# Kernel optimization log

Measured on AMD Instinct MI355X. Metric: run time of the kernel, lower is better.

## Reference

```python
import jax, jax.numpy as jnp
import numpy as np

NUM_HEADS = 8

def setup_inputs() -> dict:
    key = jax.random.key(0)
    ks = jax.random.split(key, 7)
    B, S, H = 2, 4096, 512
    sc = 1.0 / np.sqrt(H)
    x = jax.random.normal(ks[0], (B, S, H), dtype=jnp.float32)
    Wq = jax.random.normal(ks[1], (H, H), dtype=jnp.float32) * sc
    bq = jnp.zeros((H,), dtype=jnp.float32)
    Wk = jax.random.normal(ks[2], (H, H), dtype=jnp.float32) * sc
    bk = jnp.zeros((H,), dtype=jnp.float32)
    Wv = jax.random.normal(ks[3], (H, H), dtype=jnp.float32) * sc
    bv = jnp.zeros((H,), dtype=jnp.float32)
    return {"x": x, "Wq": Wq, "bq": bq, "Wk": Wk, "bk": bk, "Wv": Wv, "bv": bv}

def reference(x, Wq, bq, Wk, bk, Wv, bv):
    B, S, H = x.shape
    hd = H // NUM_HEADS
    def split_heads(t):  # [B,S,H] -> [B,nh,S,hd]
        return t.reshape(B, S, NUM_HEADS, hd).transpose(0, 2, 1, 3)
    q = split_heads(x @ Wq + bq)
    k = split_heads(x @ Wk + bk)
    v = split_heads(x @ Wv + bv)
    scores = jnp.einsum('bhqd,bhkd->bhqk', q, k) / jnp.sqrt(jnp.float32(hd))
    attn = jax.nn.softmax(scores, axis=-1)  # dropout is identity at inference
    out = jnp.einsum('bhqk,bhkd->bhqd', attn, v)
    return out.transpose(0, 2, 1, 3).reshape(B, S, H)
```

## Files before the change

### kernel.cpp

```cpp
#include <hip/hip_runtime.h>
#include <hip/hip_bf16.h>

typedef __attribute__((ext_vector_type(8))) short short8;
typedef __attribute__((ext_vector_type(4))) float float4v;
typedef __attribute__((ext_vector_type(16))) float f32x16;

using bf16 = __hip_bfloat16;

#define QSCALE 0.18033688011112042f

__device__ inline float fexp2(float x) { return __builtin_amdgcn_exp2f(x); }

__device__ inline short f2bf(float f) {
  __hip_bfloat16 h = __float2bfloat16(f);
  short s;
  __builtin_memcpy(&s, &h, 2);
  return s;
}

__device__ inline float4v mfma16(short8 a, short8 b, float4v c) {
  return __builtin_amdgcn_mfma_f32_16x16x32_bf16(a, b, c, 0, 0, 0);
}
__device__ inline f32x16 mfma32(short8 a, short8 b, f32x16 c) {
  return __builtin_amdgcn_mfma_f32_32x32x16_bf16(a, b, c, 0, 0, 0);
}
__device__ inline unsigned pk2(float lo, float hi) {
  __hip_bfloat16 l = __float2bfloat16(lo), h = __float2bfloat16(hi);
  unsigned short ls, hs;
  __builtin_memcpy(&ls, &l, 2);
  __builtin_memcpy(&hs, &h, 2);
  return (unsigned)ls | ((unsigned)hs << 16);
}


__global__ __launch_bounds__(256) void conv_x_kernel(const float* __restrict__ x,
                                                     bf16* __restrict__ xb) {
  int i = blockIdx.x * 256 + threadIdx.x;
  const float4v* src = reinterpret_cast<const float4v*>(x);
  float4v a = src[(size_t)i * 2];
  float4v c = src[(size_t)i * 2 + 1];
  short8 o;
  o[0] = f2bf(a[0]); o[1] = f2bf(a[1]); o[2] = f2bf(a[2]); o[3] = f2bf(a[3]);
  o[4] = f2bf(c[0]); o[5] = f2bf(c[1]); o[6] = f2bf(c[2]); o[7] = f2bf(c[3]);
  *reinterpret_cast<short8*>(xb + (size_t)i * 8) = o;
}

__global__ void conv_w_kernel(const float* __restrict__ Wq, const float* __restrict__ Wk,
                              const float* __restrict__ Wv, bf16* __restrict__ wt) {
  __shared__ float tile[32][33];
  int z = blockIdx.z;
  const float* W = (z == 0) ? Wq : (z == 1) ? Wk : Wv;
  int n = blockIdx.x * 32 + threadIdx.x;
  int k = blockIdx.y * 32 + threadIdx.y;
  tile[threadIdx.y][threadIdx.x] = W[(size_t)k * 512 + n];
  __syncthreads();
  int nn = blockIdx.x * 32 + threadIdx.y;
  int kk = blockIdx.y * 32 + threadIdx.x;
  wt[(size_t)z * 512 * 512 + (size_t)nn * 512 + kk] = __float2bfloat16(tile[threadIdx.x][threadIdx.y]);
}


__global__ __launch_bounds__(256) void qkv_gemm_kernel(
    const bf16* __restrict__ xb, const bf16* __restrict__ wt,
    const float* __restrict__ bq, const float* __restrict__ bk, const float* __restrict__ bv,
    bf16* __restrict__ qb, bf16* __restrict__ kbuf, bf16* __restrict__ vt) {
  __shared__ bf16 Xs[64][72];
  __shared__ bf16 Ws[64][72];
  const int m0 = blockIdx.x * 64;
  const int n0 = blockIdx.y * 64;
  const int z  = blockIdx.z;
  const bf16* W = wt + (size_t)z * 512 * 512;
  const float* bias = (z == 0) ? bq : (z == 1) ? bk : bv;
  const int t = threadIdx.x;
  const int lane = t & 63, wv = t >> 6;
  const int row = t >> 3, col8 = (t & 7) * 8;
  const int lo = lane & 15, g8 = (lane >> 4) * 8;
  float4v acc[4] = {};
  for (int k0 = 0; k0 < 512; k0 += 64) {
    *reinterpret_cast<short8*>(&Xs[row][col8])      = *reinterpret_cast<const short8*>(&xb[(size_t)(m0 + row) * 512 + k0 + col8]);
    *reinterpret_cast<short8*>(&Xs[row + 32][col8]) = *reinterpret_cast<const short8*>(&xb[(size_t)(m0 + row + 32) * 512 + k0 + col8]);
    *reinterpret_cast<short8*>(&Ws[row][col8])      = *reinterpret_cast<const short8*>(&W[(size_t)(n0 + row) * 512 + k0 + col8]);
    *reinterpret_cast<short8*>(&Ws[row + 32][col8]) = *reinterpret_cast<const short8*>(&W[(size_t)(n0 + row + 32) * 512 + k0 + col8]);
    __syncthreads();
    short8 a0 = *reinterpret_cast<const short8*>(&Xs[wv * 16 + lo][g8]);
    short8 a1 = *reinterpret_cast<const short8*>(&Xs[wv * 16 + lo][32 + g8]);
#pragma unroll
    for (int nt = 0; nt < 4; ++nt) {
      short8 b0 = *reinterpret_cast<const short8*>(&Ws[nt * 16 + lo][g8]);
      short8 b1 = *reinterpret_cast<const short8*>(&Ws[nt * 16 + lo][32 + g8]);
      acc[nt] = mfma16(a0, b0, acc[nt]);
      acc[nt] = mfma16(a1, b1, acc[nt]);
    }
    __syncthreads();
  }
#pragma unroll
  for (int nt = 0; nt < 4; ++nt) {
    int ncol = n0 + nt * 16 + lo;
    float bias_v = bias[ncol];
    int h = ncol >> 6, d = ncol & 63;
#pragma unroll
    for (int r = 0; r < 4; ++r) {
      int mrow = m0 + wv * 16 + (lane >> 4) * 4 + r;
      int bb = mrow >> 12, s = mrow & 4095;
      float v = acc[nt][r] + bias_v;
      size_t base = (size_t)(bb * 8 + h) * 262144;
      if (z == 2) {
        size_t idx = (size_t)((d >> 5) * 256 + (s >> 4)) * 512 + (d & 31) * 8 + ((s >> 3) & 1) * 256 + (s & 7);
        vt[base + idx] = __float2bfloat16(v);
      } else {
        size_t idx = (size_t)((s >> 5) * 4 + (d >> 4)) * 512 + (s & 31) * 8 + ((d >> 3) & 1) * 256 + (d & 7);
        if (z == 0) qb[base + idx] = __float2bfloat16(v * QSCALE);
        else        kbuf[base + idx] = __float2bfloat16(v);
      }
    }
  }
}


__device__ __forceinline__ void load_tiles(const bf16* __restrict__ kb2, const bf16* __restrict__ vb2,
                                           int tl, short8 (&kf)[2][4], short8 (&vf)[2][4]) {
#pragma unroll
  for (int c = 0; c < 2; ++c)
#pragma unroll
    for (int ds = 0; ds < 4; ++ds)
      kf[c][ds] = *reinterpret_cast<const short8*>(kb2 + ((size_t)(tl * 2 + c) * 4 + ds) * 512);
#pragma unroll
  for (int dt = 0; dt < 2; ++dt)
#pragma unroll
    for (int gs = 0; gs < 4; ++gs)
      vf[dt][gs] = *reinterpret_cast<const short8*>(vb2 + (size_t)(dt * 256 + tl * 4 + gs) * 512);
}

__device__ __forceinline__ void attn_step(const short8 (&kf)[2][4], const short8 (&vf)[2][4],
                                          const short8 (&qf)[4], f32x16& ot0, f32x16& ot1,
                                          float& l_run, int half) {
  f32x16 p0 = {}, p1 = {};
#pragma unroll
  for (int ds = 0; ds < 4; ++ds) {
    p0 = mfma32(kf[0][ds], qf[ds], p0);
    p1 = mfma32(kf[1][ds], qf[ds], p1);
  }

  float s0 = 0.f, s1 = 0.f, s2 = 0.f, s3 = 0.f;
#pragma unroll
  for (int r = 0; r < 16; r += 4) {
    p0[r]     = fexp2(p0[r]);     s0 += p0[r];
    p0[r + 1] = fexp2(p0[r + 1]); s1 += p0[r + 1];
    p0[r + 2] = fexp2(p0[r + 2]); s2 += p0[r + 2];
    p0[r + 3] = fexp2(p0[r + 3]); s3 += p0[r + 3];
  }
#pragma unroll
  for (int r = 0; r < 16; r += 4) {
    p1[r]     = fexp2(p1[r]);     s0 += p1[r];
    p1[r + 1] = fexp2(p1[r + 1]); s1 += p1[r + 1];
    p1[r + 2] = fexp2(p1[r + 2]); s2 += p1[r + 2];
    p1[r + 3] = fexp2(p1[r + 3]); s3 += p1[r + 3];
  }
  l_run += (s0 + s1) + (s2 + s3);

  unsigned pa[2][2][4];
#pragma unroll
  for (int c = 0; c < 2; ++c) {
    const f32x16& pc = c ? p1 : p0;
    unsigned w[4][2];
#pragma unroll
    for (int cq = 0; cq < 4; ++cq) {
      w[cq][0] = pk2(pc[4 * cq],     pc[4 * cq + 1]);
      w[cq][1] = pk2(pc[4 * cq + 2], pc[4 * cq + 3]);
    }
#pragma unroll
    for (int s = 0; s < 2; ++s)
#pragma unroll
      for (int x = 0; x < 2; ++x) {
        unsigned u = w[2 * s][x], v = w[2 * s + 1][x];
        unsigned pu = __shfl_xor(u, 32), pv = __shfl_xor(v, 32);
        pa[c][s][x]     = half ? pv : u;
        pa[c][s][2 + x] = half ? v  : pu;
      }
  }

#pragma unroll
  for (int c = 0; c < 2; ++c)
#pragma unroll
    for (int s = 0; s < 2; ++s) {
      short8 pb;
      __builtin_memcpy(&pb, pa[c][s], 16);
      ot0 = mfma32(vf[0][c * 2 + s], pb, ot0);
      ot1 = mfma32(vf[1][c * 2 + s], pb, ot1);
    }
}

__global__ __launch_bounds__(256, 1) void attn_kernel(
    const bf16* __restrict__ qbuf, const bf16* __restrict__ kbuf,
    const bf16* __restrict__ vtbuf, float* __restrict__ out) {
  int bid = blockIdx.x;
  int sw = (bid & 7) * 32 + (bid >> 3);
  int bh = sw >> 4, qt = sw & 15;
  const int bI = bh >> 3, hh = bh & 7;
  const int t = threadIdx.x;
  const int wid = t >> 6, lane = t & 63;
  const int l31 = lane & 31, half = lane >> 5;
  const int q0 = qt * 256 + wid * 64;

  const bf16* kb2 = kbuf + (size_t)bh * 262144 + lane * 8;
  const bf16* vb2 = vtbuf + (size_t)bh * 262144 + lane * 8;

  short8 qf0[4], qf1[4];
#pragma unroll
  for (int ds = 0; ds < 4; ++ds) {
    qf0[ds] = *reinterpret_cast<const short8*>(qbuf + (size_t)bh * 262144 + (size_t)(((q0 >> 5) + 0) * 4 + ds) * 512 + lane * 8);
    qf1[ds] = *reinterpret_cast<const short8*>(qbuf + (size_t)bh * 262144 + (size_t)(((q0 >> 5) + 1) * 4 + ds) * 512 + lane * 8);
  }

  f32x16 oa0 = {}, oa1 = {}, ob0 = {}, ob1 = {};
  float lA = 0.f, lB = 0.f;

  short8 kfA[2][4], vfA[2][4], kfB[2][4], vfB[2][4];
  load_tiles(kb2, vb2, 0, kfA, vfA);
  for (int it = 0; it < 64; it += 2) {
    load_tiles(kb2, vb2, it + 1, kfB, vfB);
    attn_step(kfA, vfA, qf0, oa0, oa1, lA, half);
    attn_step(kfA, vfA, qf1, ob0, ob1, lB, half);
    load_tiles(kb2, vb2, (it + 2) & 63, kfA, vfA);
    attn_step(kfB, vfB, qf0, oa0, oa1, lA, half);
    attn_step(kfB, vfB, qf1, ob0, ob1, lB, half);
  }

  lA += __shfl_xor(lA, 32);
  lB += __shfl_xor(lB, 32);

  float invA = 1.0f / lA, invB = 1.0f / lB;
#pragma unroll
  for (int set = 0; set < 2; ++set) {
    const f32x16& t0 = set ? ob0 : oa0;
    const f32x16& t1 = set ? ob1 : oa1;
    float inv = set ? invB : invA;
    int q = q0 + set * 32 + l31;
    float* obase = out + ((size_t)bI * 4096 + q) * 512 + hh * 64;
#pragma unroll
    for (int cq = 0; cq < 4; ++cq) {
      float4v o0, o1;
#pragma unroll
      for (int rr = 0; rr < 4; ++rr) {
        o0[rr] = t0[4 * cq + rr] * inv;
        o1[rr] = t1[4 * cq + rr] * inv;
      }
      *reinterpret_cast<float4v*>(obase + 8 * cq + 4 * half) = o0;
      *reinterpret_cast<float4v*>(obase + 32 + 8 * cq + 4 * half) = o1;
    }
  }
}


extern "C" void kernel_launch(void* const* d_in, const int* in_sizes, int n_in,
                              void* d_out, int out_size, void* d_ws, size_t ws_size,
                              hipStream_t stream) {
  const float* x  = (const float*)d_in[0];
  const float* Wq = (const float*)d_in[1];
  const float* bq = (const float*)d_in[2];
  const float* Wk = (const float*)d_in[3];
  const float* bk = (const float*)d_in[4];
  const float* Wv = (const float*)d_in[5];
  const float* bv = (const float*)d_in[6];
  float* out = (float*)d_out;

  char* ws = (char*)d_ws;
  bf16* xb = (bf16*)(ws + 0);
  bf16* wt = (bf16*)(ws + 8388608);
  bf16* qb = (bf16*)(ws + 9961472);
  bf16* kb = (bf16*)(ws + 18350080);
  bf16* vt = (bf16*)(ws + 26738688);

  conv_x_kernel<<<2048, 256, 0, stream>>>(x, xb);
  conv_w_kernel<<<dim3(16, 16, 3), dim3(32, 32), 0, stream>>>(Wq, Wk, Wv, wt);
  qkv_gemm_kernel<<<dim3(128, 8, 3), 256, 0, stream>>>(xb, wt, bq, bk, bv, qb, kb, vt);
  attn_kernel<<<256, 256, 0, stream>>>(qb, kb, vt, out);
}
```

Baseline: 146.8 us.

## Stage K/V tiles through LDS with double-buffered direct global-to-LDS loads

Replaces per-wave redundant global loads of K and V tiles with a cooperative staging scheme: each of the four waves copies a quarter of the tile into shared memory using global_load_lds, double-buffered across iterations with a barrier per tile. Waves then read fragments from LDS. This aims to cut the fourfold redundant L2/global traffic per block. It adds LDS read traffic and a block-wide barrier every tile, and the previous register-level prefetch of the next tile is dropped.

Measured after the change: 171.7 us. +16.9%, slower.

```diff
diff --git a/kernel.cpp b/kernel.cpp
--- a/kernel.cpp
+++ b/kernel.cpp
@@ -117,20 +117,6 @@
 }
 
 
-__device__ __forceinline__ void load_tiles(const bf16* __restrict__ kb2, const bf16* __restrict__ vb2,
-                                           int tl, short8 (&kf)[2][4], short8 (&vf)[2][4]) {
-#pragma unroll
-  for (int c = 0; c < 2; ++c)
-#pragma unroll
-    for (int ds = 0; ds < 4; ++ds)
-      kf[c][ds] = *reinterpret_cast<const short8*>(kb2 + ((size_t)(tl * 2 + c) * 4 + ds) * 512);
-#pragma unroll
-  for (int dt = 0; dt < 2; ++dt)
-#pragma unroll
-    for (int gs = 0; gs < 4; ++gs)
-      vf[dt][gs] = *reinterpret_cast<const short8*>(vb2 + (size_t)(dt * 256 + tl * 4 + gs) * 512);
-}
-
 __device__ __forceinline__ void attn_step(const short8 (&kf)[2][4], const short8 (&vf)[2][4],
                                           const short8 (&qf)[4], f32x16& ot0, f32x16& ot1,
                                           float& l_run, int half) {
@@ -193,6 +179,7 @@
 __global__ __launch_bounds__(256, 1) void attn_kernel(
     const bf16* __restrict__ qbuf, const bf16* __restrict__ kbuf,
     const bf16* __restrict__ vtbuf, float* __restrict__ out) {
+  __shared__ __align__(16) bf16 smem[2][8192];
   int bid = blockIdx.x;
   int sw = (bid & 7) * 32 + (bid >> 3);
   int bh = sw >> 4, qt = sw & 15;
@@ -202,8 +189,8 @@
   const int l31 = lane & 31, half = lane >> 5;
   const int q0 = qt * 256 + wid * 64;
 
-  const bf16* kb2 = kbuf + (size_t)bh * 262144 + lane * 8;
-  const bf16* vb2 = vtbuf + (size_t)bh * 262144 + lane * 8;
+  const bf16* kb = kbuf + (size_t)bh * 262144;
+  const bf16* vb = vtbuf + (size_t)bh * 262144;
 
   short8 qf0[4], qf1[4];
 #pragma unroll
@@ -212,18 +199,48 @@
     qf1[ds] = *reinterpret_cast<const short8*>(qbuf + (size_t)bh * 262144 + (size_t)(((q0 >> 5) + 1) * 4 + ds) * 512 + lane * 8);
   }
 
+  auto stage = [&](int tile, int buf) {
+    const bf16* s;
+    if (wid == 0)      s = kb + (size_t)tile * 4096;
+    else if (wid == 1) s = kb + (size_t)tile * 4096 + 2048;
+    else if (wid == 2) s = vb + (size_t)tile * 2048;
+    else               s = vb + 131072 + (size_t)tile * 2048;
+    s += lane * 8;
+    bf16* d = &smem[buf][wid * 2048];
+#pragma unroll
+    for (int c2 = 0; c2 < 4; ++c2)
+      __builtin_amdgcn_global_load_lds(
+          (const __attribute__((address_space(1))) void*)(s + c2 * 512),
+          (__attribute__((address_space(3))) void*)(d + c2 * 512),
+          16, 0, 0);
+  };
+
   f32x16 oa0 = {}, oa1 = {}, ob0 = {}, ob1 = {};
   float lA = 0.f, lB = 0.f;
 
-  short8 kfA[2][4], vfA[2][4], kfB[2][4], vfB[2][4];
-  load_tiles(kb2, vb2, 0, kfA, vfA);
-  for (int it = 0; it < 64; it += 2) {
-    load_tiles(kb2, vb2, it + 1, kfB, vfB);
-    attn_step(kfA, vfA, qf0, oa0, oa1, lA, half);
-    attn_step(kfA, vfA, qf1, ob0, ob1, lB, half);
-    load_tiles(kb2, vb2, (it + 2) & 63, kfA, vfA);
-    attn_step(kfB, vfB, qf0, oa0, oa1, lA, half);
-    attn_step(kfB, vfB, qf1, ob0, ob1, lB, half);
+  stage(0, 0);
+  __syncthreads();
+
+  for (int tl = 0; tl < 64; ++tl) {
+    int cur = tl & 1;
+    stage((tl + 1) & 63, cur ^ 1);
+
+    short8 kf[2][4], vf[2][4];
+#pragma unroll
+    for (int c = 0; c < 2; ++c)
+#pragma unroll
+      for (int ds = 0; ds < 4; ++ds)
+        kf[c][ds] = *reinterpret_cast<const short8*>(&smem[cur][(c * 4 + ds) * 512 + lane * 8]);
+#pragma unroll
+    for (int dt = 0; dt < 2; ++dt)
+#pragma unroll
+      for (int gs = 0; gs < 4; ++gs)
+        vf[dt][gs] = *reinterpret_cast<const short8*>(&smem[cur][4096 + dt * 2048 + gs * 512 + lane * 8]);
+
+    attn_step(kf, vf, qf0, oa0, oa1, lA, half);
+    attn_step(kf, vf, qf1, ob0, ob1, lB, half);
+
+    __syncthreads();
   }
 
   lA += __shfl_xor(lA, 32);
```

## Permute K row layout so P accumulator feeds PV MFMA without lane shuffles

Applied to the files above, without the earlier changes.

The projection kernel now writes K with a permuted sequence order inside each 32-row block. With that order, the 32x32 MFMA score accumulator already sits in the register layout the P·V MFMA B operand expects. This removes the cross-half __shfl_xor exchanges and selects from the attention inner loop, trading a slightly more complex index computation in the K store. Correctness depends on the permutation matching both the MFMA output layout and the V layout exactly.

After: 124.0 us. -15.6%, faster.

```diff
diff --git a/kernel.cpp b/kernel.cpp
--- a/kernel.cpp
+++ b/kernel.cpp
@@ -107,10 +107,15 @@
       if (z == 2) {
         size_t idx = (size_t)((d >> 5) * 256 + (s >> 4)) * 512 + (d & 31) * 8 + ((s >> 3) & 1) * 256 + (s & 7);
         vt[base + idx] = __float2bfloat16(v);
+      } else if (z == 0) {
+        size_t idx = (size_t)((s >> 5) * 4 + (d >> 4)) * 512 + (s & 31) * 8 + ((d >> 3) & 1) * 256 + (d & 7);
+        qb[base + idx] = __float2bfloat16(v * QSCALE);
       } else {
-        size_t idx = (size_t)((s >> 5) * 4 + (d >> 4)) * 512 + (s & 31) * 8 + ((d >> 3) & 1) * 256 + (d & 7);
-        if (z == 0) qb[base + idx] = __float2bfloat16(v * QSCALE);
-        else        kbuf[base + idx] = __float2bfloat16(v);
+        int s31 = s & 31, b = s31 >> 2;
+        int nb = (b & 4) | ((b & 1) << 1) | ((b >> 1) & 1);
+        int sp = (nb << 2) | (s31 & 3);
+        size_t idx = (size_t)((s >> 5) * 4 + (d >> 4)) * 512 + sp * 8 + ((d >> 3) & 1) * 256 + (d & 7);
+        kbuf[base + idx] = __float2bfloat16(v);
       }
     }
   }
@@ -133,7 +138,7 @@
 
 __device__ __forceinline__ void attn_step(const short8 (&kf)[2][4], const short8 (&vf)[2][4],
                                           const short8 (&qf)[4], f32x16& ot0, f32x16& ot1,
-                                          float& l_run, int half) {
+                                          float& l_run) {
   f32x16 p0 = {}, p1 = {};
 #pragma unroll
   for (int ds = 0; ds < 4; ++ds) {
@@ -158,36 +163,22 @@
   }
   l_run += (s0 + s1) + (s2 + s3);
 
-  unsigned pa[2][2][4];
 #pragma unroll
   for (int c = 0; c < 2; ++c) {
     const f32x16& pc = c ? p1 : p0;
-    unsigned w[4][2];
-#pragma unroll
-    for (int cq = 0; cq < 4; ++cq) {
-      w[cq][0] = pk2(pc[4 * cq],     pc[4 * cq + 1]);
-      w[cq][1] = pk2(pc[4 * cq + 2], pc[4 * cq + 3]);
-    }
-#pragma unroll
-    for (int s = 0; s < 2; ++s)
-#pragma unroll
-      for (int x = 0; x < 2; ++x) {
-        unsigned u = w[2 * s][x], v = w[2 * s + 1][x];
-        unsigned pu = __shfl_xor(u, 32), pv = __shfl_xor(v, 32);
-        pa[c][s][x]     = half ? pv : u;
-        pa[c][s][2 + x] = half ? v  : pu;
-      }
-  }
-
-#pragma unroll
-  for (int c = 0; c < 2; ++c)
 #pragma unroll
     for (int s = 0; s < 2; ++s) {
+      unsigned arr[4];
+      arr[0] = pk2(pc[8 * s],     pc[8 * s + 1]);
+      arr[1] = pk2(pc[8 * s + 2], pc[8 * s + 3]);
+      arr[2] = pk2(pc[8 * s + 4], pc[8 * s + 5]);
+      arr[3] = pk2(pc[8 * s + 6], pc[8 * s + 7]);
       short8 pb;
-      __builtin_memcpy(&pb, pa[c][s], 16);
+      __builtin_memcpy(&pb, arr, 16);
       ot0 = mfma32(vf[0][c * 2 + s], pb, ot0);
       ot1 = mfma32(vf[1][c * 2 + s], pb, ot1);
     }
+  }
 }
 
 __global__ __launch_bounds__(256, 1) void attn_kernel(
@@ -219,11 +210,11 @@
   load_tiles(kb2, vb2, 0, kfA, vfA);
   for (int it = 0; it < 64; it += 2) {
     load_tiles(kb2, vb2, it + 1, kfB, vfB);
-    attn_step(kfA, vfA, qf0, oa0, oa1, lA, half);
-    attn_step(kfA, vfA, qf1, ob0, ob1, lB, half);
+    attn_step(kfA, vfA, qf0, oa0, oa1, lA);
+    attn_step(kfA, vfA, qf1, ob0, ob1, lB);
     load_tiles(kb2, vb2, (it + 2) & 63, kfA, vfA);
-    attn_step(kfB, vfB, qf0, oa0, oa1, lA, half);
-    attn_step(kfB, vfB, qf1, ob0, ob1, lB, half);
+    attn_step(kfB, vfB, qf0, oa0, oa1, lA);
+    attn_step(kfB, vfB, qf1, ob0, ob1, lB);
   }
 
   lA += __shfl_xor(lA, 32);
```
